# Kernel optimization log

Measured on AMD Instinct MI355X. Metric: run time of the kernel, lower is better.

The kernel has to match this reference:

```python
import jax, jax.numpy as jnp
import numpy as np

WIN = (8, 7, 7)
SHIFT = (4, 3, 3)
HEADS = 4
DIM = 128
VOL = WIN[0] * WIN[1] * WIN[2]  # 392


def _rel_index():
    coords = np.stack(np.meshgrid(np.arange(WIN[0]), np.arange(WIN[1]), np.arange(WIN[2]), indexing='ij'))
    cf = coords.reshape(3, -1)
    rel = (cf[:, :, None] - cf[:, None, :]).transpose(1, 2, 0).astype(np.int64)
    rel[..., 0] += WIN[0] - 1
    rel[..., 1] += WIN[1] - 1
    rel[..., 2] += WIN[2] - 1
    rel[..., 0] *= (2 * WIN[1] - 1) * (2 * WIN[2] - 1)
    rel[..., 1] *= 2 * WIN[2] - 1
    return rel.sum(-1)  # [VOL, VOL]


def _attn_mask(tp, hp, wp):
    m = np.zeros((tp, hp, wp))
    slices = [((0, -WIN[i]), (-WIN[i], -SHIFT[i]), (-SHIFT[i], None)) for i in range(3)]
    cnt = 0
    for d in slices[0]:
        for h in slices[1]:
            for w in slices[2]:
                m[d[0]:d[1], h[0]:h[1], w[0]:w[1]] = cnt
                cnt += 1
    m = m.reshape(tp // WIN[0], WIN[0], hp // WIN[1], WIN[1], wp // WIN[2], WIN[2])
    m = m.transpose(0, 2, 4, 1, 3, 5).reshape(-1, VOL)  # [nW, VOL]
    diff = m[:, None, :] - m[:, :, None]
    return np.where(diff != 0, -100.0, 0.0).astype(np.float32)  # [nW, VOL, VOL]


_REL_IDX = _rel_index()


def setup_inputs() -> dict:
    key = jax.random.key(0)
    ks = jax.random.split(key, 6)
    return {
        'x': jax.random.normal(ks[0], (2, 16, 56, 56, DIM), dtype=jnp.float32),
        'qkv_weight': jax.random.normal(ks[1], (3 * DIM, DIM), dtype=jnp.float32) * 0.02,
        'qkv_bias': jax.random.normal(ks[2], (3 * DIM,), dtype=jnp.float32) * 0.02,
        'proj_weight': jax.random.normal(ks[3], (DIM, DIM), dtype=jnp.float32) * 0.02,
        'proj_bias': jax.random.normal(ks[4], (DIM,), dtype=jnp.float32) * 0.02,
        'rel_bias_table': jax.random.normal(ks[5], ((2 * WIN[0] - 1) * (2 * WIN[1] - 1) * (2 * WIN[2] - 1), HEADS), dtype=jnp.float32) * 0.02,
    }


def reference(x, qkv_weight, qkv_bias, proj_weight, proj_bias, rel_bias_table):
    b, t, h, w, c = x.shape
    hd = c // HEADS
    nt, nh, nw = t // WIN[0], h // WIN[1], w // WIN[2]
    NW = nt * nh * nw

    # relative position bias: [1, HEADS, VOL, VOL]
    bias = rel_bias_table[jnp.asarray(_REL_IDX.flatten())]
    bias = bias.reshape(VOL, VOL, HEADS).transpose(2, 0, 1)[None]

    # cyclic shift
    xs = jnp.roll(x, shift=(-SHIFT[0], -SHIFT[1], -SHIFT[2]), axis=(1, 2, 3))

    # window partition -> [B*NW, VOL, C]
    xw = xs.reshape(b, nt, WIN[0], nh, WIN[1], nw, WIN[2], c)
    xw = xw.transpose(0, 1, 3, 5, 2, 4, 6, 7).reshape(b * NW, VOL, c)

    qkv = xw @ qkv_weight.T + qkv_bias
    qkv = qkv.reshape(b * NW, VOL, 3, HEADS, hd).transpose(2, 0, 3, 1, 4)
    q, k, v = qkv[0] * (hd ** -0.5), qkv[1], qkv[2]

    attn = jnp.einsum('nhqd,nhkd->nhqk', q, k) + bias
    mask = jnp.asarray(_attn_mask(t, h, w))  # [NW, VOL, VOL]
    attn = attn.reshape(b, NW, HEADS, VOL, VOL) + mask[None, :, None]
    attn = jax.nn.softmax(attn, axis=-1).reshape(b * NW, HEADS, VOL, VOL)

    out = jnp.einsum('nhqk,nhkd->nqhd', attn, v).reshape(b * NW, VOL, c)
    out = out @ proj_weight.T + proj_bias

    # window reverse
    out = out.reshape(b, nt, nh, nw, WIN[0], WIN[1], WIN[2], c)
    out = out.transpose(0, 1, 4, 2, 5, 3, 6, 7).reshape(b, t, h, w, c)
    out = jnp.roll(out, shift=SHIFT, axis=(1, 2, 3))
    return out
```

## Files before the change

kernel.cpp:

```cpp
#include <hip/hip_runtime.h>


#define DIMC   128
#define HEADS  4
#define HD     32
#define VOL    392
#define VPAD   416
#define TQ     400
#define TK     416
#define SCALE2 0.25503490443f
#define LOG2E  1.4426950408889634f
#define MASK2  144.26950408889634f

typedef __bf16 bf16;
typedef __attribute__((ext_vector_type(8))) __bf16 bf16x8;
typedef __attribute__((ext_vector_type(4))) __bf16 bf16x4;
typedef __attribute__((ext_vector_type(4))) float  f32x4;

#define OFF_Q   0
#define OFF_K   (392*32)
#define OFF_VT  (2*392*32)
#define VTCOLS  416
#define LDS_ELEMS (2*392*32 + 32*VTCOLS)
#define SMEM_A  (LDS_ELEMS*2)
#define AW_BYTES (256ull * VPAD * DIMC * 2ull)

static __device__ inline bf16x8 pack8(float4 a, float4 b) {
    bf16x8 r;
    r[0] = (bf16)a.x; r[1] = (bf16)a.y; r[2] = (bf16)a.z; r[3] = (bf16)a.w;
    r[4] = (bf16)b.x; r[5] = (bf16)b.y; r[6] = (bf16)b.z; r[7] = (bf16)b.w;
    return r;
}
static __device__ inline bf16x8 zero8() {
    bf16x8 z;
#pragma unroll
    for (int i = 0; i < 8; ++i) z[i] = (bf16)0.0f;
    return z;
}
static __device__ inline int swz4(int row) { return ((row >> 1) ^ (row >> 3)) & 3; }

static __device__ inline unsigned pkbf(float a, float b) {
    unsigned short ua = __builtin_bit_cast(unsigned short, (bf16)a);
    unsigned short ub = __builtin_bit_cast(unsigned short, (bf16)b);
    return (unsigned)ua | ((unsigned)ub << 16);
}

#if defined(__has_builtin)
#if __has_builtin(__builtin_amdgcn_exp2f)
#define HAS_EXP2 1
#endif
#endif
static __device__ inline float exp2_hw(float x) {
#ifdef HAS_EXP2
    return __builtin_amdgcn_exp2f(x);
#else
    float r; asm volatile("v_exp_f32 %0, %1\n\ts_nop 0" : "=v"(r) : "v"(x)); return r;
#endif
}

__global__ __launch_bounds__(256) void gen_table(const float* __restrict__ btab,
                                                 bf16* __restrict__ tbl) {
    const int idx = blockIdx.x * 256 + threadIdx.x;
    const int total = 8 * HEADS * TQ * (TK / 4);
    if (idx >= total) return;
    const int k4  = (idx % (TK / 4)) * 4;
    const int q   = (idx / (TK / 4)) % TQ;
    const int h   = (idx / ((TK / 4) * TQ)) & 3;
    const int pat = idx / ((TK / 4) * TQ * HEADS);
    const int tb = (pat >> 2) & 1, hb = (pat >> 1) & 1, wb = pat & 1;

    int qt = 0, qh = 0, qw = 0, lq = 0;
    if (q < VOL) {
        qt = q / 49; const int qr = q - qt * 49; qh = qr / 7; qw = qr - qh * 7;
        lq = (tb ? (qt < 4 ? 1 : 2) : 0) * 9 + (hb ? (qh < 4 ? 1 : 2) : 0) * 3 +
             (wb ? (qw < 4 ? 1 : 2) : 0);
    }
    bf16x4 out;
#pragma unroll
    for (int j = 0; j < 4; ++j) {
        const int k = k4 + j;
        float v;
        if (k >= VOL)      v = -30000.0f;
        else if (q >= VOL) v = 0.0f;
        else {
            const int kt = k / 49; const int kr = k - kt * 49;
            const int kh = kr / 7; const int kw = kr - kh * 7;
            const int rel = ((qt - kt + 7) * 13 + (qh - kh + 6)) * 13 + (qw - kw + 6);
            v = btab[rel * HEADS + h] * LOG2E;
            const int lk = (tb ? (kt < 4 ? 1 : 2) : 0) * 9 +
                           (hb ? (kh < 4 ? 1 : 2) : 0) * 3 +
                           (wb ? (kw < 4 ? 1 : 2) : 0);
            if (lq != lk) v -= MASK2;
        }
        out[j] = (bf16)v;
    }
    *(bf16x4*)&tbl[((size_t)(pat * HEADS + h) * TQ + q) * TK + k4] = out;
}

#define NJ 7

__global__ __attribute__((amdgpu_flat_work_group_size(256, 256),
                          amdgpu_waves_per_eu(2, 2)))
void swin_attn(
    const float* __restrict__ x, const float* __restrict__ wqkv,
    const float* __restrict__ bqkv, const bf16* __restrict__ tbl,
    bf16* __restrict__ aw)
{
    const int bid  = blockIdx.x;
    const int xcd  = bid & 7;
    const int tt   = bid >> 3;
    const int win  = xcd * 32 + (tt >> 2);
    const int head = tt & 3;
    const int b    = win >> 7;
    const int wrem = win & 127;
    const int it   = wrem >> 6;
    const int ih   = (wrem >> 3) & 7;
    const int iw   = wrem & 7;
    const int pat  = ((it == 1) ? 4 : 0) | ((ih == 7) ? 2 : 0) | ((iw == 7) ? 1 : 0);

    const int tid  = threadIdx.x;
    const int lane = tid & 63;
    const int wv   = tid >> 6;
    const int l16  = lane & 15;
    const int lg   = lane >> 4;

    extern __shared__ char smem[];
    bf16* lds = (bf16*)smem;
    const bf16* tblh = tbl + (size_t)(pat * HEADS + head) * (TQ * TK);

    bf16x8 wfr[6][4];
    float  bcol[4];
#pragma unroll
    for (int o = 0; o < 6; ++o) {
        const int g = o >> 1, h2 = o & 1;
        const int wrow = g * DIMC + head * HD + h2 * 16 + l16;
        const float* wp = wqkv + (size_t)wrow * DIMC + 8 * lg;
#pragma unroll
        for (int ks = 0; ks < 4; ++ks)
            wfr[o][ks] = pack8(*(const float4*)(wp + ks * 32),
                               *(const float4*)(wp + ks * 32 + 4));
        if (o < 4) bcol[o] = bqkv[wrow];
    }
    float bvr[2][4];
#pragma unroll
    for (int h2 = 0; h2 < 2; ++h2)
#pragma unroll
        for (int r = 0; r < 4; ++r)
            bvr[h2][r] = bqkv[2 * DIMC + head * HD + h2 * 16 + lg * 4 + r];

    for (int mt = wv; mt < 26; mt += 4) {
        const int tv = mt * 16 + l16;
        bf16x8 af[4];
        if (tv < VOL) {
            const int lt = tv / 49, rr = tv - lt * 49;
            const int lh = rr / 7,  lw = rr - lh * 7;
            const int t0 = (it * 8 + lt + 4) & 15;
            int h0 = ih * 7 + lh + 3; if (h0 >= 56) h0 -= 56;
            int w0 = iw * 7 + lw + 3; if (w0 >= 56) w0 -= 56;
            const float* xp = x + (size_t)(((b * 16 + t0) * 56 + h0) * 56 + w0) * DIMC + 8 * lg;
#pragma unroll
            for (int ks = 0; ks < 4; ++ks)
                af[ks] = pack8(*(const float4*)(xp + ks * 32),
                               *(const float4*)(xp + ks * 32 + 4));
        } else {
#pragma unroll
            for (int ks = 0; ks < 4; ++ks) af[ks] = zero8();
        }
#pragma unroll
        for (int o = 0; o < 4; ++o) {
            f32x4 acc = {0.f, 0.f, 0.f, 0.f};
#pragma unroll
            for (int ks = 0; ks < 4; ++ks)
                acc = __builtin_amdgcn_mfma_f32_16x16x32_bf16(af[ks], wfr[o][ks], acc, 0, 0, 0);
            bf16* dst = lds + ((o < 2) ? OFF_Q : OFF_K);
            const float sc = (o < 2) ? SCALE2 : 1.0f;
            const int cb = (o & 1) * 16 + l16;
#pragma unroll
            for (int r = 0; r < 4; ++r) {
                const int row = mt * 16 + lg * 4 + r;
                if (row < VOL)
                    dst[row * 32 + (cb ^ (swz4(row) << 3))] = (bf16)((acc[r] + bcol[o]) * sc);
            }
        }
#pragma unroll
        for (int h2 = 0; h2 < 2; ++h2) {
            f32x4 acc = {0.f, 0.f, 0.f, 0.f};
#pragma unroll
            for (int ks = 0; ks < 4; ++ks)
                acc = __builtin_amdgcn_mfma_f32_16x16x32_bf16(wfr[4 + h2][ks], af[ks], acc, 0, 0, 0);
#pragma unroll
            for (int r = 0; r < 4; ++r) {
                const int n = h2 * 16 + lg * 4 + r;
                lds[OFF_VT + n * VTCOLS + (tv ^ (swz4(n) << 3))] = (bf16)(acc[r] + bvr[h2][r]);
            }
        }
    }
    __syncthreads();

    {
        const int c = l16 & 3, d = l16 >> 2;
        const int rowA  = c + 8 * d;
        const int swzA  = (c >> 1) ^ d;
        const int swzB  = (2 + (c >> 1)) ^ d;
        const int kbA   = OFF_K + rowA * 32       + ((lg * 8) ^ (swzA << 3));
        const int kbB   = OFF_K + (rowA + 4) * 32 + ((lg * 8) ^ (swzB << 3));
        const int vb0   = OFF_VT + l16 * VTCOLS        + ((lg * 8) ^ (swz4(l16) << 3));
        const int vb1   = OFF_VT + (16 + l16) * VTCOLS + ((lg * 8) ^ (swz4(16 + l16) << 3));

        bf16x8 qf[NJ];
        const bf16* tbp[NJ];
        f32x4  o0[NJ], o1[NJ];
        float  sum[NJ];
#pragma unroll
        for (int j = 0; j < NJ; ++j) {
            const int mt   = wv + 4 * j;
            const int qtok = mt * 16 + l16;
            const int qr   = (qtok < VOL) ? qtok : (VOL - 1);
            const int qc   = (qtok < TQ)  ? qtok : (TQ - 1);
            qf[j] = *(const bf16x8*)&lds[OFF_Q + qr * 32 + ((lg * 8) ^ (swz4(qr) << 3))];
            tbp[j] = tblh + qc * TK + 8 * lg;
            o0[j] = f32x4{0.f, 0.f, 0.f, 0.f};
            o1[j] = f32x4{0.f, 0.f, 0.f, 0.f};
            sum[j] = 0.f;
        }

        uint4 bufA[NJ], bufB[NJ];
#pragma unroll
        for (int j = 0; j < NJ; ++j) bufA[j] = *(const uint4*)(tbp[j]);

#define CH_BODY(CH, CUR)                                                      \
        {                                                                     \
            const int ch = (CH);                                              \
            const bf16x8 kfA = *(const bf16x8*)&lds[kbA + ch * 1024];         \
            const bf16x8 kfB = *(const bf16x8*)&lds[kbB + ch * 1024];         \
            const bf16x8 v0  = *(const bf16x8*)&lds[vb0 + ch * 32];           \
            const bf16x8 v1  = *(const bf16x8*)&lds[vb1 + ch * 32];           \
            _Pragma("unroll")                                                 \
            for (int j = 0; j < NJ; ++j) {                                    \
                if (wv + 4 * j < 25) {                                        \
                    const uint4 bu = CUR[j];                                  \
                    f32x4 cA, cB;                                             \
                    cA[0] = __builtin_bit_cast(float, bu.x << 16);            \
                    cA[1] = __builtin_bit_cast(float, bu.x & 0xffff0000u);    \
                    cA[2] = __builtin_bit_cast(float, bu.y << 16);            \
                    cA[3] = __builtin_bit_cast(float, bu.y & 0xffff0000u);    \
                    cB[0] = __builtin_bit_cast(float, bu.z << 16);            \
                    cB[1] = __builtin_bit_cast(float, bu.z & 0xffff0000u);    \
                    cB[2] = __builtin_bit_cast(float, bu.w << 16);            \
                    cB[3] = __builtin_bit_cast(float, bu.w & 0xffff0000u);    \
                    const f32x4 sA = __builtin_amdgcn_mfma_f32_16x16x32_bf16(kfA, qf[j], cA, 0, 0, 0); \
                    const f32x4 sB = __builtin_amdgcn_mfma_f32_16x16x32_bf16(kfB, qf[j], cB, 0, 0, 0); \
                    float pA[4], pB[4];                                       \
                    _Pragma("unroll")                                         \
                    for (int r = 0; r < 4; ++r) {                             \
                        pA[r] = exp2_hw(sA[r]);                               \
                        pB[r] = exp2_hw(sB[r]);                               \
                        sum[j] += pA[r] + pB[r];                              \
                    }                                                         \
                    union { unsigned u[4]; bf16x8 v; } pw;                    \
                    pw.u[0] = pkbf(pA[0], pA[1]); pw.u[1] = pkbf(pA[2], pA[3]); \
                    pw.u[2] = pkbf(pB[0], pB[1]); pw.u[3] = pkbf(pB[2], pB[3]); \
                    o0[j] = __builtin_amdgcn_mfma_f32_16x16x32_bf16(v0, pw.v, o0[j], 0, 0, 0); \
                    o1[j] = __builtin_amdgcn_mfma_f32_16x16x32_bf16(v1, pw.v, o1[j], 0, 0, 0); \
                }                                                             \
            }                                                                 \
        }
#define CH_PRE(CH, DST)                                                       \
        {                                                                     \
            const int chp_ = (CH) < 12 ? (CH) : 12;                           \
            _Pragma("unroll")                                                 \
            for (int j = 0; j < NJ; ++j)                                      \
                DST[j] = *(const uint4*)(tbp[j] + chp_ * 32);                 \
        }

#pragma unroll 1
        for (int chp = 0; chp < 12; chp += 2) {
            CH_PRE(chp + 1, bufB)
            CH_BODY(chp, bufA)
            CH_PRE(chp + 2, bufA)
            CH_BODY(chp + 1, bufB)
        }
        CH_BODY(12, bufA)
#undef CH_BODY
#undef CH_PRE

#pragma unroll
        for (int j = 0; j < NJ; ++j) {
            const int mt   = wv + 4 * j;
            const int qtok = mt * 16 + l16;
            if (mt < 25) {
                float s = sum[j];
                s += __shfl_xor(s, 16);
                s += __shfl_xor(s, 32);
                const float inv = 1.0f / s;
                if (qtok < VOL) {
                    bf16x4 w0, w1;
#pragma unroll
                    for (int r = 0; r < 4; ++r) {
                        w0[r] = (bf16)(o0[j][r] * inv);
                        w1[r] = (bf16)(o1[j][r] * inv);
                    }
                    bf16* op = aw + ((size_t)win * VPAD + qtok) * DIMC + head * HD + lg * 4;
                    *(bf16x4*)op = w0;
                    *(bf16x4*)(op + 16) = w1;
                }
            }
        }
    }
}

__global__ __launch_bounds__(256, 2) void swin_proj(
    const bf16* __restrict__ aw, const float* __restrict__ wproj,
    const float* __restrict__ bproj, float* __restrict__ out)
{
    const int bid  = blockIdx.x;
    const int xcd  = bid & 7;
    const int rest = bid >> 3;
    const int win  = xcd * 32 + (rest & 31);
    const int half = rest >> 5;
    const int b    = win >> 7;
    const int wrem = win & 127;
    const int it   = wrem >> 6;
    const int ih   = (wrem >> 3) & 7;
    const int iw   = wrem & 7;

    const int tid  = threadIdx.x;
    const int lane = tid & 63;
    const int wid  = tid >> 6;
    const int l16  = lane & 15;
    const int lg   = lane >> 4;

    const int mt_end = half ? 25 : 13;
    for (int mt = 13 * half + wid; mt < mt_end; mt += 4) {
        bf16x8 af[4];
        const bf16* ap = aw + ((size_t)win * VPAD + mt * 16 + l16) * DIMC + 8 * lg;
#pragma unroll
        for (int ks = 0; ks < 4; ++ks) af[ks] = *(const bf16x8*)(ap + ks * 32);

        float* ob[4]; bool qok[4];
#pragma unroll
        for (int r = 0; r < 4; ++r) {
            int q = mt * 16 + lg * 4 + r;
            qok[r] = q < VOL; if (!qok[r]) q = 0;
            const int lt = q / 49, rr = q - lt * 49;
            const int lh = rr / 7, lw = rr - lh * 7;
            const int t0 = (it * 8 + lt + 4) & 15;
            int h0 = ih * 7 + lh + 3; if (h0 >= 56) h0 -= 56;
            int w0 = iw * 7 + lw + 3; if (w0 >= 56) w0 -= 56;
            ob[r] = out + (size_t)(((b * 16 + t0) * 56 + h0) * 56 + w0) * DIMC;
        }
#pragma unroll
        for (int nt = 0; nt < 8; ++nt) {
            f32x4 acc = {0.f, 0.f, 0.f, 0.f};
            const float* wp = wproj + (size_t)(nt * 16 + l16) * DIMC + 8 * lg;
#pragma unroll
            for (int ks = 0; ks < 4; ++ks) {
                float4 u0 = *(const float4*)(wp + ks * 32);
                float4 u1 = *(const float4*)(wp + ks * 32 + 4);
                acc = __builtin_amdgcn_mfma_f32_16x16x32_bf16(af[ks], pack8(u0, u1), acc, 0, 0, 0);
            }
            const float bv = bproj[nt * 16 + l16];
#pragma unroll
            for (int r = 0; r < 4; ++r)
                if (qok[r]) ob[r][nt * 16 + l16] = acc[r] + bv;
        }
    }
}

extern "C" void kernel_launch(void* const* d_in, const int* in_sizes, int n_in,
                              void* d_out, int out_size, void* d_ws, size_t ws_size,
                              hipStream_t stream) {
    const float* x     = (const float*)d_in[0];
    const float* wqkv  = (const float*)d_in[1];
    const float* bqkv  = (const float*)d_in[2];
    const float* wproj = (const float*)d_in[3];
    const float* bproj = (const float*)d_in[4];
    const float* btab  = (const float*)d_in[5];
    bf16*  aw  = (bf16*)d_ws;
    bf16*  tbl = (bf16*)((char*)d_ws + AW_BYTES);
    float* out = (float*)d_out;

    (void)hipFuncSetAttribute((const void*)swin_attn,
                              hipFuncAttributeMaxDynamicSharedMemorySize, SMEM_A);

    const int tbl_threads = 8 * HEADS * TQ * (TK / 4);
    gen_table<<<dim3((tbl_threads + 255) / 256), dim3(256), 0, stream>>>(btab, tbl);
    swin_attn<<<dim3(1024), dim3(256), SMEM_A, stream>>>(x, wqkv, bqkv, tbl, aw);
    swin_proj<<<dim3(512), dim3(256), 0, stream>>>(aw, wproj, bproj, out);
}
```

Before: 132.6 us.

## Alias Q and K in LDS and raise waves per EU for occupancy

Each wave now writes its Q tile and immediately loads it into registers, before the K projection for that tile overwrites the same LDS region. This removes the separate Q buffer and shrinks LDS per block from about 77 KB to about 52 KB. With the smaller footprint the launch bound goes from 2 to 3 waves per EU, and the dynamic-shared-memory attribute call is dropped. The risk is that the tighter register budget, with Q fragments now held live across the projection loop, causes spills.

```diff
diff --git a/kernel.cpp b/kernel.cpp
--- a/kernel.cpp
+++ b/kernel.cpp
@@ -17,11 +17,9 @@
 typedef __attribute__((ext_vector_type(4))) __bf16 bf16x4;
 typedef __attribute__((ext_vector_type(4))) float  f32x4;
 
-#define OFF_Q   0
-#define OFF_K   (392*32)
-#define OFF_VT  (2*392*32)
+#define OFF_VT  (392*32)
 #define VTCOLS  416
-#define LDS_ELEMS (2*392*32 + 32*VTCOLS)
+#define LDS_ELEMS (392*32 + 32*VTCOLS)
 #define SMEM_A  (LDS_ELEMS*2)
 #define AW_BYTES (256ull * VPAD * DIMC * 2ull)
 
@@ -100,7 +98,7 @@
 #define NJ 7
 
 __global__ __attribute__((amdgpu_flat_work_group_size(256, 256),
-                          amdgpu_waves_per_eu(2, 2)))
+                          amdgpu_waves_per_eu(3, 3)))
 void swin_attn(
     const float* __restrict__ x, const float* __restrict__ wqkv,
     const float* __restrict__ bqkv, const bf16* __restrict__ tbl,
@@ -148,6 +146,8 @@
         for (int r = 0; r < 4; ++r)
             bvr[h2][r] = bqkv[2 * DIMC + head * HD + h2 * 16 + lg * 4 + r];
 
+    bf16x8 qf[NJ] = {};
+
     for (int mt = wv; mt < 26; mt += 4) {
         const int tv = mt * 16 + l16;
         bf16x8 af[4];
@@ -167,19 +167,35 @@
             for (int ks = 0; ks < 4; ++ks) af[ks] = zero8();
         }
 #pragma unroll
-        for (int o = 0; o < 4; ++o) {
+        for (int o = 0; o < 2; ++o) {
             f32x4 acc = {0.f, 0.f, 0.f, 0.f};
 #pragma unroll
             for (int ks = 0; ks < 4; ++ks)
                 acc = __builtin_amdgcn_mfma_f32_16x16x32_bf16(af[ks], wfr[o][ks], acc, 0, 0, 0);
-            bf16* dst = lds + ((o < 2) ? OFF_Q : OFF_K);
-            const float sc = (o < 2) ? SCALE2 : 1.0f;
             const int cb = (o & 1) * 16 + l16;
 #pragma unroll
             for (int r = 0; r < 4; ++r) {
                 const int row = mt * 16 + lg * 4 + r;
                 if (row < VOL)
-                    dst[row * 32 + (cb ^ (swz4(row) << 3))] = (bf16)((acc[r] + bcol[o]) * sc);
+                    lds[row * 32 + (cb ^ (swz4(row) << 3))] = (bf16)((acc[r] + bcol[o]) * SCALE2);
+            }
+        }
+        if (mt < 25) {
+            const int qr = (tv < VOL) ? tv : (VOL - 1);
+            qf[(mt - wv) >> 2] = *(const bf16x8*)&lds[qr * 32 + ((lg * 8) ^ (swz4(qr) << 3))];
+        }
+#pragma unroll
+        for (int o = 2; o < 4; ++o) {
+            f32x4 acc = {0.f, 0.f, 0.f, 0.f};
+#pragma unroll
+            for (int ks = 0; ks < 4; ++ks)
+                acc = __builtin_amdgcn_mfma_f32_16x16x32_bf16(af[ks], wfr[o][ks], acc, 0, 0, 0);
+            const int cb = (o & 1) * 16 + l16;
+#pragma unroll
+            for (int r = 0; r < 4; ++r) {
+                const int row = mt * 16 + lg * 4 + r;
+                if (row < VOL)
+                    lds[row * 32 + (cb ^ (swz4(row) << 3))] = (bf16)(acc[r] + bcol[o]);
             }
         }
 #pragma unroll
@@ -202,22 +218,18 @@
         const int rowA  = c + 8 * d;
         const int swzA  = (c >> 1) ^ d;
         const int swzB  = (2 + (c >> 1)) ^ d;
-        const int kbA   = OFF_K + rowA * 32       + ((lg * 8) ^ (swzA << 3));
-        const int kbB   = OFF_K + (rowA + 4) * 32 + ((lg * 8) ^ (swzB << 3));
+        const int kbA   = rowA * 32       + ((lg * 8) ^ (swzA << 3));
+        const int kbB   = (rowA + 4) * 32 + ((lg * 8) ^ (swzB << 3));
         const int vb0   = OFF_VT + l16 * VTCOLS        + ((lg * 8) ^ (swz4(l16) << 3));
         const int vb1   = OFF_VT + (16 + l16) * VTCOLS + ((lg * 8) ^ (swz4(16 + l16) << 3));
 
-        bf16x8 qf[NJ];
         const bf16* tbp[NJ];
         f32x4  o0[NJ], o1[NJ];
         float  sum[NJ];
 #pragma unroll
         for (int j = 0; j < NJ; ++j) {
-            const int mt   = wv + 4 * j;
-            const int qtok = mt * 16 + l16;
-            const int qr   = (qtok < VOL) ? qtok : (VOL - 1);
-            const int qc   = (qtok < TQ)  ? qtok : (TQ - 1);
-            qf[j] = *(const bf16x8*)&lds[OFF_Q + qr * 32 + ((lg * 8) ^ (swz4(qr) << 3))];
+            const int qtok = (wv + 4 * j) * 16 + l16;
+            const int qc   = (qtok < TQ) ? qtok : (TQ - 1);
             tbp[j] = tblh + qc * TK + 8 * lg;
             o0[j] = f32x4{0.f, 0.f, 0.f, 0.f};
             o1[j] = f32x4{0.f, 0.f, 0.f, 0.f};
@@ -380,9 +392,6 @@
     bf16*  tbl = (bf16*)((char*)d_ws + AW_BYTES);
     float* out = (float*)d_out;
 
-    (void)hipFuncSetAttribute((const void*)swin_attn,
-                              hipFuncAttributeMaxDynamicSharedMemorySize, SMEM_A);
-
     const int tbl_threads = 8 * HEADS * TQ * (TK / 4);
     gen_table<<<dim3((tbl_threads + 255) / 256), dim3(256), 0, stream>>>(btab, tbl);
     swin_attn<<<dim3(1024), dim3(256), SMEM_A, stream>>>(x, wqkv, bqkv, tbl, aw);
```

Result: slower. 343.7 us (+159.2%).
